# Performance work log

Hardware: AMD Instinct MI355X
Metric: run time of the kernel (lower is better)

The kernel has to match this reference:

```python
import jax, jax.numpy as jnp
import numpy as np

B, N, H = 4, 512, 64


def setup_inputs() -> dict:
    key = jax.random.key(0)
    ks = jax.random.split(key, 20)
    s = 0.05
    inp = {
        "positions": jax.random.uniform(ks[0], (B, N, 2), dtype=jnp.float32) * 10.0,
        "box_size": 10,
        # encoder: Linear(2,H) -> ReLU -> Linear(H,H)
        "enc_w1": jax.random.normal(ks[1], (2, H), jnp.float32) * s,
        "enc_b1": jnp.zeros((H,), jnp.float32),
        "enc_w2": jax.random.normal(ks[2], (H, H), jnp.float32) * s,
        "enc_b2": jnp.zeros((H,), jnp.float32),
        # message: Linear(2H+1,H) -> ReLU -> Linear(H,H)
        "msg_w1": jax.random.normal(ks[3], (2 * H + 1, H), jnp.float32) * s,
        "msg_b1": jnp.zeros((H,), jnp.float32),
        "msg_w2": jax.random.normal(ks[4], (H, H), jnp.float32) * s,
        "msg_b2": jnp.zeros((H,), jnp.float32),
        # update: Linear(2H,H) -> ReLU -> Linear(H,H)
        "upd_w1": jax.random.normal(ks[5], (2 * H, H), jnp.float32) * s,
        "upd_b1": jnp.zeros((H,), jnp.float32),
        "upd_w2": jax.random.normal(ks[6], (H, H), jnp.float32) * s,
        "upd_b2": jnp.zeros((H,), jnp.float32),
        # decoder: Linear(H,H) -> ReLU -> Linear(H,2)
        "dec_w1": jax.random.normal(ks[7], (H, H), jnp.float32) * s,
        "dec_b1": jnp.zeros((H,), jnp.float32),
        "dec_w2": jax.random.normal(ks[8], (H, 2), jnp.float32) * s,
        "dec_b2": jnp.zeros((2,), jnp.float32),
    }
    return inp


def reference(positions, box_size, enc_w1, enc_b1, enc_w2, enc_b2,
              msg_w1, msg_b1, msg_w2, msg_b2,
              upd_w1, upd_b1, upd_w2, upd_b2,
              dec_w1, dec_b1, dec_w2, dec_b2):
    box = jnp.float32(box_size)
    n = positions.shape[1]

    # encoder
    h = jax.nn.relu(positions @ enc_w1 + enc_b1) @ enc_w2 + enc_b2  # (B,N,H)

    # pairwise PBC displacement: r[b,i,j] = pos_j - pos_i (minimum image)
    r = positions[:, None, :, :] - positions[:, :, None, :]  # (B,N,N,2)
    r = r - box * jnp.round(r / box)
    dist = jnp.linalg.norm(r, axis=-1, keepdims=True)  # (B,N,N,1)

    # message MLP layer 1 without materializing concat: split msg_w1 rows
    w_i, w_j, w_d = msg_w1[:h.shape[-1]], msg_w1[h.shape[-1]:2 * h.shape[-1]], msg_w1[2 * h.shape[-1]:]
    a_i = h @ w_i  # (B,N,H) depends only on receiver i
    a_j = h @ w_j  # (B,N,H) depends only on sender j
    pre = a_i[:, :, None, :] + a_j[:, None, :, :] + dist * w_d[0] + msg_b1  # (B,N,N,H)
    m = jax.nn.relu(pre) @ msg_w2 + msg_b2  # (B,N,N,H)

    # mean over j != i
    mask = (1.0 - jnp.eye(n, dtype=m.dtype))[None, :, :, None]
    agg = jnp.sum(m * mask, axis=2) / jnp.float32(n - 1)  # (B,N,H)

    u_in = jnp.concatenate([h, agg], axis=-1)  # (B,N,2H)
    u = jax.nn.relu(u_in @ upd_w1 + upd_b1) @ upd_w2 + upd_b2
    forces = jax.nn.relu(u @ dec_w1 + dec_b1) @ dec_w2 + dec_b2  # (B,N,2)
    return forces
```

## Files before the change

### kernel.cpp

```cpp
#include <hip/hip_runtime.h>

#define BB 4
#define NN 512
#define HH 64
#define NODES (BB*NN)
#define NSL 8
#define JCH (NN/NSL)
#define TI 4

typedef float v4f __attribute__((ext_vector_type(4)));

__global__ __launch_bounds__(256) void enc_kernel(
    const float* __restrict__ pos,
    const float* __restrict__ enc_w1, const float* __restrict__ enc_b1,
    const float* __restrict__ enc_w2, const float* __restrict__ enc_b2,
    const float* __restrict__ msg_w1,
    float* __restrict__ h_out, float* __restrict__ ai_out, float* __restrict__ aj_out)
{
    const int w = threadIdx.x >> 6;
    const int k = threadIdx.x & 63;
    const int node = blockIdx.x*4 + w;
    __shared__ float t_s[4][HH];
    __shared__ float h_s[4][HH];

    const float px = pos[node*2+0];
    const float py = pos[node*2+1];

    float t = fmaf(px, enc_w1[k], fmaf(py, enc_w1[HH + k], enc_b1[k]));
    t_s[w][k] = fmaxf(t, 0.f);
    __syncthreads();

    float h = enc_b2[k];
    #pragma unroll
    for (int m = 0; m < HH; ++m) h = fmaf(t_s[w][m], enc_w2[m*HH + k], h);
    h_s[w][k] = h;
    h_out[node*HH + k] = h;
    __syncthreads();

    float aiv = 0.f, ajv = 0.f;
    #pragma unroll
    for (int m = 0; m < HH; ++m) {
        const float hm = h_s[w][m];
        aiv = fmaf(hm, msg_w1[m*HH + k],        aiv);
        ajv = fmaf(hm, msg_w1[(HH + m)*HH + k], ajv);
    }
    ai_out[node*HH + k] = aiv;
    aj_out[node*HH + k] = ajv;
}

__global__ __launch_bounds__(512, 2) void pairout_kernel(
    const float* __restrict__ pos, const int* __restrict__ box_ptr,
    const float* __restrict__ msg_w1, const float* __restrict__ msg_b1,
    const float* __restrict__ ai, const float* __restrict__ aj,
    const float* __restrict__ h_in,
    const float* __restrict__ msg_w2, const float* __restrict__ msg_b2,
    const float* __restrict__ upd_w1, const float* __restrict__ upd_b1,
    const float* __restrict__ upd_w2, const float* __restrict__ upd_b2,
    const float* __restrict__ dec_w1, const float* __restrict__ dec_b1,
    const float* __restrict__ dec_w2, const float* __restrict__ dec_b2,
    float* __restrict__ out)
{
    const int w  = threadIdx.x >> 6;
    const int l  = threadIdx.x & 63;
    const int jgrp = l >> 4;
    const int kq   = l & 15;
    const int ig = blockIdx.x;
    const int b  = ig >> 7;
    const int i0 = (ig & 127) * TI;
    const int node0 = b*NN + i0;
    const int jch0  = w * JCH;

    __shared__ float dbuf[NSL][TI*64];
    __shared__ float acc_lds[NSL][TI][HH];
    __shared__ float A [TI][HH];
    __shared__ float Hs[TI][HH];
    __shared__ float G [TI][HH];
    __shared__ float P [TI][HH];
    __shared__ float U [TI][HH];
    __shared__ float D [TI][HH];

    {
        const float box  = (float)box_ptr[0];
        const float hbox = 0.5f * box;
        const float2* pos2 = (const float2*)pos;
        float* db = dbuf[w];

        const v4f wd4 = *(const v4f*)(msg_w1 + 2*HH*HH + 4*kq);
        const v4f b1  = *(const v4f*)(msg_b1 + 4*kq);
        v4f base4[TI];
        float2 pi[TI];
        #pragma unroll
        for (int ii = 0; ii < TI; ++ii) {
            base4[ii] = *(const v4f*)(ai + (size_t)(node0 + ii)*HH + 4*kq) + b1;
            pi[ii] = pos2[node0 + ii];
        }

        {
            const float2 pj = pos2[b*NN + jch0 + l];
            #pragma unroll
            for (int ii = 0; ii < TI; ++ii) {
                float dx = pj.x - pi[ii].x;
                float dy = pj.y - pi[ii].y;
                dx -= (dx >  hbox) ? box : 0.f;
                dx += (dx < -hbox) ? box : 0.f;
                dy -= (dy >  hbox) ? box : 0.f;
                dy += (dy < -hbox) ? box : 0.f;
                db[ii*64 + (l&3)*16 + (l>>2)] = sqrtf(fmaf(dx, dx, dy*dy));
            }
        }
        __builtin_amdgcn_wave_barrier();

        v4f acc[TI];
        #pragma unroll
        for (int ii = 0; ii < TI; ++ii) acc[ii] = (v4f){0.f,0.f,0.f,0.f};

        #pragma unroll
        for (int t4 = 0; t4 < 4; ++t4) {
            v4f d4[TI];
            #pragma unroll
            for (int ii = 0; ii < TI; ++ii)
                d4[ii] = *(const v4f*)(db + ii*64 + jgrp*16 + 4*t4);
            #pragma unroll
            for (int u = 0; u < 4; ++u) {
                const int o = (t4*4 + u)*4 + jgrp;
                const v4f a4 = *(const v4f*)(aj + (size_t)(b*NN + jch0 + o)*HH + 4*kq);
                #pragma unroll
                for (int ii = 0; ii < TI; ++ii) {
                    const float d = d4[ii][u];
                    v4f t = __builtin_elementwise_fma((v4f)(d), wd4, a4 + base4[ii]);
                    acc[ii] += __builtin_elementwise_max(t, (v4f){0.f,0.f,0.f,0.f});
                }
            }
        }

        #pragma unroll
        for (int ii = 0; ii < TI; ++ii) {
            #pragma unroll
            for (int c = 0; c < 4; ++c) {
                float v = acc[ii][c];
                v += __shfl_xor(v, 16, 64);
                v += __shfl_xor(v, 32, 64);
                acc[ii][c] = v;
            }
        }

        {
            const int ii = jgrp;
            const int i  = i0 + ii;
            v4f a = acc[ii];
            if ((i >> 6) == w) {
                const v4f ajs = *(const v4f*)(aj + (size_t)(b*NN + i)*HH + 4*kq);
                a -= __builtin_elementwise_max(base4[ii] + ajs, (v4f){0.f,0.f,0.f,0.f});
            }
            *(v4f*)(&acc_lds[w][ii][4*kq]) = a;
        }
    }
    __syncthreads();

    if (w < 4) {
        float a = 0.f;
        #pragma unroll
        for (int s = 0; s < NSL; ++s) a += acc_lds[s][w][l];
        A[w][l] = a;
    } else {
        const int nn = w - 4;
        Hs[nn][l] = h_in[(size_t)(node0 + nn)*HH + l];
    }
    __syncthreads();

    const int nn  = w & 3;
    const int o   = w >> 2;
    const int jg8 = l >> 3;
    const int kq8 = l & 7;
    const int ocol = o*32 + 4*kq8;
    const float inv = 1.f / (float)(NN - 1);

    {
        v4f q = {0.f,0.f,0.f,0.f};
        #pragma unroll
        for (int mm = 0; mm < 8; ++mm) {
            const int m = 8*mm + jg8;
            const v4f wrow = *(const v4f*)(msg_w2 + m*HH + ocol);
            q = __builtin_elementwise_fma((v4f)(A[nn][m]), wrow, q);
        }
        #pragma unroll
        for (int c = 0; c < 4; ++c) {
            float x = q[c];
            x += __shfl_xor(x, 8, 64);
            x += __shfl_xor(x, 16, 64);
            x += __shfl_xor(x, 32, 64);
            q[c] = x;
        }
        q = __builtin_elementwise_fma(q, (v4f)(inv), *(const v4f*)(msg_b2 + ocol));
        if (jg8 == 0) *(v4f*)(&G[nn][ocol]) = q;
    }
    __syncthreads();

    {
        v4f q = {0.f,0.f,0.f,0.f};
        #pragma unroll
        for (int mm = 0; mm < 8; ++mm) {
            const int m = 8*mm + jg8;
            const v4f wrow = *(const v4f*)(upd_w1 + m*HH + ocol);
            q = __builtin_elementwise_fma((v4f)(Hs[nn][m]), wrow, q);
        }
        #pragma unroll
        for (int mm = 0; mm < 8; ++mm) {
            const int m = 8*mm + jg8;
            const v4f wrow = *(const v4f*)(upd_w1 + (size_t)(HH + m)*HH + ocol);
            q = __builtin_elementwise_fma((v4f)(G[nn][m]), wrow, q);
        }
        #pragma unroll
        for (int c = 0; c < 4; ++c) {
            float x = q[c];
            x += __shfl_xor(x, 8, 64);
            x += __shfl_xor(x, 16, 64);
            x += __shfl_xor(x, 32, 64);
            q[c] = x;
        }
        q = __builtin_elementwise_max(q + *(const v4f*)(upd_b1 + ocol),
                                      (v4f){0.f,0.f,0.f,0.f});
        if (jg8 == 0) *(v4f*)(&P[nn][ocol]) = q;
    }
    __syncthreads();

    {
        v4f q = {0.f,0.f,0.f,0.f};
        #pragma unroll
        for (int mm = 0; mm < 8; ++mm) {
            const int m = 8*mm + jg8;
            const v4f wrow = *(const v4f*)(upd_w2 + m*HH + ocol);
            q = __builtin_elementwise_fma((v4f)(P[nn][m]), wrow, q);
        }
        #pragma unroll
        for (int c = 0; c < 4; ++c) {
            float x = q[c];
            x += __shfl_xor(x, 8, 64);
            x += __shfl_xor(x, 16, 64);
            x += __shfl_xor(x, 32, 64);
            q[c] = x;
        }
        q = q + *(const v4f*)(upd_b2 + ocol);
        if (jg8 == 0) *(v4f*)(&U[nn][ocol]) = q;
    }
    __syncthreads();

    {
        v4f q = {0.f,0.f,0.f,0.f};
        #pragma unroll
        for (int mm = 0; mm < 8; ++mm) {
            const int m = 8*mm + jg8;
            const v4f wrow = *(const v4f*)(dec_w1 + m*HH + ocol);
            q = __builtin_elementwise_fma((v4f)(U[nn][m]), wrow, q);
        }
        #pragma unroll
        for (int c = 0; c < 4; ++c) {
            float x = q[c];
            x += __shfl_xor(x, 8, 64);
            x += __shfl_xor(x, 16, 64);
            x += __shfl_xor(x, 32, 64);
            q[c] = x;
        }
        q = __builtin_elementwise_max(q + *(const v4f*)(dec_b1 + ocol),
                                      (v4f){0.f,0.f,0.f,0.f});
        if (jg8 == 0) *(v4f*)(&D[nn][ocol]) = q;
    }
    __syncthreads();

    if (w < 4) {
        const float d = D[w][l];
        float f0 = d * dec_w2[2*l + 0];
        float f1 = d * dec_w2[2*l + 1];
        #pragma unroll
        for (int off = 32; off >= 1; off >>= 1) {
            f0 += __shfl_xor(f0, off, 64);
            f1 += __shfl_xor(f1, off, 64);
        }
        if (l == 0) {
            out[(size_t)(node0 + w)*2 + 0] = f0 + dec_b2[0];
            out[(size_t)(node0 + w)*2 + 1] = f1 + dec_b2[1];
        }
    }
}

extern "C" void kernel_launch(void* const* d_in, const int* in_sizes, int n_in,
                              void* d_out, int out_size, void* d_ws, size_t ws_size,
                              hipStream_t stream) {
    const float* pos    = (const float*)d_in[0];
    const int*   boxp   = (const int*)  d_in[1];
    const float* enc_w1 = (const float*)d_in[2];
    const float* enc_b1 = (const float*)d_in[3];
    const float* enc_w2 = (const float*)d_in[4];
    const float* enc_b2 = (const float*)d_in[5];
    const float* msg_w1 = (const float*)d_in[6];
    const float* msg_b1 = (const float*)d_in[7];
    const float* msg_w2 = (const float*)d_in[8];
    const float* msg_b2 = (const float*)d_in[9];
    const float* upd_w1 = (const float*)d_in[10];
    const float* upd_b1 = (const float*)d_in[11];
    const float* upd_w2 = (const float*)d_in[12];
    const float* upd_b2 = (const float*)d_in[13];
    const float* dec_w1 = (const float*)d_in[14];
    const float* dec_b1 = (const float*)d_in[15];
    const float* dec_w2 = (const float*)d_in[16];
    const float* dec_b2 = (const float*)d_in[17];

    float* ws = (float*)d_ws;
    float* h  = ws;
    float* ai = ws + (size_t)NODES*HH;
    float* aj = ws + (size_t)2*NODES*HH;

    enc_kernel<<<NODES/4, 256, 0, stream>>>(pos, enc_w1, enc_b1, enc_w2, enc_b2,
                                            msg_w1, h, ai, aj);
    pairout_kernel<<<NODES/TI, 512, 0, stream>>>(pos, boxp, msg_w1, msg_b1,
                                                 ai, aj, h,
                                                 msg_w2, msg_b2,
                                                 upd_w1, upd_b1, upd_w2, upd_b2,
                                                 dec_w1, dec_b1, dec_w2, dec_b2,
                                                 (float*)d_out);
}
```

Before: 26.92 us.

## Fuse encoder and pair kernels into one cooperative kernel with grid sync

Merges the encoder and the pairwise message/update/decoder kernels into a single cooperative launch of 256 blocks of 512 threads, each block owning 8 nodes. A grid-wide sync separates the encoder phase, which writes aj to global memory, from the pair phase; h and ai stay in LDS. The change removes one kernel launch and the global round-trip for h and ai, at the cost of a grid barrier, per-call host occupancy queries, and a cooperative launch that falls back to the old two-kernel path if it fails.

Measured after the change: 27.13 us. About the same (+0.8%).

```diff
diff --git a/kernel.cpp b/kernel.cpp
--- a/kernel.cpp
+++ b/kernel.cpp
@@ -1,14 +1,216 @@
 #include <hip/hip_runtime.h>
+#include <hip/hip_cooperative_groups.h>
+
+namespace cg = cooperative_groups;
 
 #define BB 4
 #define NN 512
 #define HH 64
 #define NODES (BB*NN)
+#define TB 8
+#define NBLK (NODES/TB)
 #define NSL 8
 #define JCH (NN/NSL)
 #define TI 4
 
 typedef float v4f __attribute__((ext_vector_type(4)));
+
+__global__ __launch_bounds__(512, 2) void fused_kernel(
+    const float* __restrict__ pos, const int* __restrict__ box_ptr,
+    const float* __restrict__ enc_w1, const float* __restrict__ enc_b1,
+    const float* __restrict__ enc_w2, const float* __restrict__ enc_b2,
+    const float* __restrict__ msg_w1, const float* __restrict__ msg_b1,
+    const float* __restrict__ msg_w2, const float* __restrict__ msg_b2,
+    const float* __restrict__ upd_w1, const float* __restrict__ upd_b1,
+    const float* __restrict__ upd_w2, const float* __restrict__ upd_b2,
+    const float* __restrict__ dec_w1, const float* __restrict__ dec_b1,
+    const float* __restrict__ dec_w2, const float* __restrict__ dec_b2,
+    float* __restrict__ aj_g, float* __restrict__ out)
+{
+    const int w = threadIdx.x >> 6;
+    const int l = threadIdx.x & 63;
+    const int ig = blockIdx.x;
+    const int b  = ig >> 6;
+    const int i0l = (ig & 63) * TB;
+    const int node0 = b*NN + i0l;
+
+    __shared__ float dbuf[8][256];
+    __shared__ float acc_lds[8][4][HH];
+    __shared__ float t_s [TB][HH];
+    __shared__ float Hs  [TB][HH];
+    __shared__ float ai_s[TB][HH];
+    __shared__ float aj_s[TB][HH];
+    __shared__ float A   [TB][HH];
+    __shared__ float G   [TB][HH];
+    __shared__ float P   [TB][HH];
+    __shared__ float U   [TB][HH];
+
+    {
+        const int node = node0 + w;
+        const float px = pos[node*2+0];
+        const float py = pos[node*2+1];
+        float t = fmaf(px, enc_w1[l], fmaf(py, enc_w1[HH + l], enc_b1[l]));
+        t_s[w][l] = fmaxf(t, 0.f);
+        __builtin_amdgcn_wave_barrier();
+
+        float h = enc_b2[l];
+        #pragma unroll
+        for (int m = 0; m < HH; ++m) h = fmaf(t_s[w][m], enc_w2[m*HH + l], h);
+        Hs[w][l] = h;
+        __builtin_amdgcn_wave_barrier();
+
+        float aiv = 0.f, ajv = 0.f;
+        #pragma unroll
+        for (int m = 0; m < HH; ++m) {
+            const float hm = Hs[w][m];
+            aiv = fmaf(hm, msg_w1[m*HH + l],        aiv);
+            ajv = fmaf(hm, msg_w1[(HH + m)*HH + l], ajv);
+        }
+        ai_s[w][l] = aiv;
+        aj_s[w][l] = ajv;
+        aj_g[(size_t)node*HH + l] = ajv;
+    }
+
+    __threadfence();
+    cg::this_grid().sync();
+    __threadfence();
+
+    {
+        const int jgrp = l >> 4;
+        const int kq   = l & 15;
+        const int q  = w & 1;
+        const int jh = w >> 1;
+
+        const float box  = (float)box_ptr[0];
+        const float hbox = 0.5f * box;
+        const float2* pos2 = (const float2*)pos;
+        float* db = dbuf[w];
+
+        const v4f wd4 = *(const v4f*)(msg_w1 + 2*HH*HH + 4*kq);
+        const v4f b1q = *(const v4f*)(msg_b1 + 4*kq);
+        v4f base4[4];
+        float2 pi[4];
+        #pragma unroll
+        for (int ii = 0; ii < 4; ++ii) {
+            base4[ii] = *(const v4f*)(&ai_s[q*4 + ii][4*kq]) + b1q;
+            pi[ii] = pos2[node0 + q*4 + ii];
+        }
+        v4f acc[4];
+        #pragma unroll
+        for (int ii = 0; ii < 4; ++ii) acc[ii] = (v4f){0.f,0.f,0.f,0.f};
+
+        #pragma unroll
+        for (int sl = 0; sl < 2; ++sl) {
+            const int j0 = (jh*2 + sl) * 64;
+            {
+                const float2 pj = pos2[b*NN + j0 + l];
+                #pragma unroll
+                for (int ii = 0; ii < 4; ++ii) {
+                    float dx = pj.x - pi[ii].x;
+                    float dy = pj.y - pi[ii].y;
+                    dx -= (dx >  hbox) ? box : 0.f;
+                    dx += (dx < -hbox) ? box : 0.f;
+                    dy -= (dy >  hbox) ? box : 0.f;
+                    dy += (dy < -hbox) ? box : 0.f;
+                    db[ii*64 + (l&3)*16 + (l>>2)] = sqrtf(fmaf(dx, dx, dy*dy));
+                }
+            }
+            __builtin_amdgcn_wave_barrier();
+
+            #pragma unroll
+            for (int t4 = 0; t4 < 4; ++t4) {
+                v4f d4[4];
+                #pragma unroll
+                for (int ii = 0; ii < 4; ++ii)
+                    d4[ii] = *(const v4f*)(db + ii*64 + jgrp*16 + 4*t4);
+                #pragma unroll
+                for (int u = 0; u < 4; ++u) {
+                    const int jo = (t4*4 + u)*4 + jgrp;
+                    const v4f a4 = *(const v4f*)(aj_g + (size_t)(b*NN + j0 + jo)*HH + 4*kq);
+                    #pragma unroll
+                    for (int ii = 0; ii < 4; ++ii) {
+                        v4f t = __builtin_elementwise_fma((v4f)(d4[ii][u]), wd4,
+                                                          a4 + base4[ii]);
+                        acc[ii] += __builtin_elementwise_max(t, (v4f){0.f,0.f,0.f,0.f});
+                    }
+                }
+            }
+            __builtin_amdgcn_wave_barrier();
+        }
+
+        #pragma unroll
+        for (int ii = 0; ii < 4; ++ii) {
+            #pragma unroll
+            for (int c = 0; c < 4; ++c) {
+                float v = acc[ii][c];
+                v += __shfl_xor(v, 16, 64);
+                v += __shfl_xor(v, 32, 64);
+                acc[ii][c] = v;
+            }
+        }
+
+        {
+            const int ii = jgrp;
+            const int il = i0l + q*4 + ii;
+            v4f a = acc[ii];
+            if ((il >> 7) == jh) {
+                const v4f ajs = *(const v4f*)(&aj_s[q*4 + ii][4*kq]);
+                a -= __builtin_elementwise_max(base4[ii] + ajs, (v4f){0.f,0.f,0.f,0.f});
+            }
+            *(v4f*)(&acc_lds[w][ii][4*kq]) = a;
+        }
+    }
+    __syncthreads();
+
+    {
+        const int q = w >> 2, ii = w & 3;
+        float a = 0.f;
+        #pragma unroll
+        for (int jh = 0; jh < 4; ++jh) a += acc_lds[jh*2 + q][ii][l];
+        A[w][l] = a;
+    }
+    __builtin_amdgcn_wave_barrier();
+
+    const float inv = 1.f / (float)(NN - 1);
+
+    float agg = 0.f;
+    #pragma unroll
+    for (int m = 0; m < HH; ++m) agg = fmaf(A[w][m], msg_w2[m*HH + l], agg);
+    agg = fmaf(agg, inv, msg_b2[l]);
+    G[w][l] = agg;
+    __builtin_amdgcn_wave_barrier();
+
+    float p = upd_b1[l];
+    #pragma unroll
+    for (int m = 0; m < HH; ++m) p = fmaf(Hs[w][m], upd_w1[m*HH + l], p);
+    #pragma unroll
+    for (int m = 0; m < HH; ++m) p = fmaf(G[w][m], upd_w1[(HH + m)*HH + l], p);
+    P[w][l] = fmaxf(p, 0.f);
+    __builtin_amdgcn_wave_barrier();
+
+    float u = upd_b2[l];
+    #pragma unroll
+    for (int m = 0; m < HH; ++m) u = fmaf(P[w][m], upd_w2[m*HH + l], u);
+    U[w][l] = u;
+    __builtin_amdgcn_wave_barrier();
+
+    float d = dec_b1[l];
+    #pragma unroll
+    for (int m = 0; m < HH; ++m) d = fmaf(U[w][m], dec_w1[m*HH + l], d);
+    d = fmaxf(d, 0.f);
+
+    float f0 = d * dec_w2[2*l + 0];
+    float f1 = d * dec_w2[2*l + 1];
+    #pragma unroll
+    for (int off = 32; off >= 1; off >>= 1) {
+        f0 += __shfl_xor(f0, off, 64);
+        f1 += __shfl_xor(f1, off, 64);
+    }
+    if (l == 0) {
+        out[(size_t)(node0 + w)*2 + 0] = f0 + dec_b2[0];
+        out[(size_t)(node0 + w)*2 + 1] = f1 + dec_b2[1];
+    }
+}
 
 __global__ __launch_bounds__(256) void enc_kernel(
     const float* __restrict__ pos,
@@ -122,8 +324,8 @@
                 d4[ii] = *(const v4f*)(db + ii*64 + jgrp*16 + 4*t4);
             #pragma unroll
             for (int u = 0; u < 4; ++u) {
-                const int o = (t4*4 + u)*4 + jgrp;
-                const v4f a4 = *(const v4f*)(aj + (size_t)(b*NN + jch0 + o)*HH + 4*kq);
+                const int jo = (t4*4 + u)*4 + jgrp;
+                const v4f a4 = *(const v4f*)(aj + (size_t)(b*NN + jch0 + jo)*HH + 4*kq);
                 #pragma unroll
                 for (int ii = 0; ii < TI; ++ii) {
                     const float d = d4[ii][u];
@@ -305,17 +507,44 @@
     const float* dec_w2 = (const float*)d_in[16];
     const float* dec_b2 = (const float*)d_in[17];
 
-    float* ws = (float*)d_ws;
-    float* h  = ws;
-    float* ai = ws + (size_t)NODES*HH;
-    float* aj = ws + (size_t)2*NODES*HH;
-
-    enc_kernel<<<NODES/4, 256, 0, stream>>>(pos, enc_w1, enc_b1, enc_w2, enc_b2,
-                                            msg_w1, h, ai, aj);
-    pairout_kernel<<<NODES/TI, 512, 0, stream>>>(pos, boxp, msg_w1, msg_b1,
-                                                 ai, aj, h,
-                                                 msg_w2, msg_b2,
-                                                 upd_w1, upd_b1, upd_w2, upd_b2,
-                                                 dec_w1, dec_b1, dec_w2, dec_b2,
-                                                 (float*)d_out);
+    float* ws   = (float*)d_ws;
+    float* h    = ws;
+    float* ai   = ws + (size_t)NODES*HH;
+    float* aj_g = ws + (size_t)2*NODES*HH;
+    float* outp = (float*)d_out;
+
+    int dev = 0;
+    (void)hipGetDevice(&dev);
+    int coop = 0;
+    (void)hipDeviceGetAttribute(&coop, hipDeviceAttributeCooperativeLaunch, dev);
+    int maxblk = 0;
+    (void)hipOccupancyMaxActiveBlocksPerMultiprocessor(&maxblk, fused_kernel, 512, 0);
+
+    bool done = false;
+    if (coop && maxblk >= 1) {
+        void* args[] = {
+            (void*)&pos, (void*)&boxp,
+            (void*)&enc_w1, (void*)&enc_b1, (void*)&enc_w2, (void*)&enc_b2,
+            (void*)&msg_w1, (void*)&msg_b1, (void*)&msg_w2, (void*)&msg_b2,
+            (void*)&upd_w1, (void*)&upd_b1, (void*)&upd_w2, (void*)&upd_b2,
+            (void*)&dec_w1, (void*)&dec_b1, (void*)&dec_w2, (void*)&dec_b2,
+            (void*)&aj_g, (void*)&outp
+        };
+        hipError_t rc = hipLaunchCooperativeKernel((const void*)fused_kernel,
+                                                   dim3(NBLK), dim3(512),
+                                                   args, 0, stream);
+        if (rc == hipSuccess) done = true;
+        else (void)hipGetLastError();
+    }
+
+    if (!done) {
+        enc_kernel<<<NODES/4, 256, 0, stream>>>(pos, enc_w1, enc_b1, enc_w2, enc_b2,
+                                                msg_w1, h, ai, aj_g);
+        pairout_kernel<<<NODES/TI, 512, 0, stream>>>(pos, boxp, msg_w1, msg_b1,
+                                                     ai, aj_g, h,
+                                                     msg_w2, msg_b2,
+                                                     upd_w1, upd_b1, upd_w2, upd_b2,
+                                                     dec_w1, dec_b1, dec_w2, dec_b2,
+                                                     outp);
+    }
 }
```
